# Optimization experiments

Measured on AMD Instinct MI355X. Metric: run time of the kernel, lower is better.

The kernel has to match this reference:

```python
import jax, jax.numpy as jnp
import numpy as np

N_ITER = 3

def setup_inputs() -> dict:
    key = jax.random.key(0)
    k1, k2 = jax.random.split(key)
    x = jax.random.normal(k1, (8, 1024, 512), dtype=jnp.float32)
    W = jax.random.normal(k2, (4, 512, 512), dtype=jnp.float32)
    return {"x": x, "W": W}

def reference(x, W):
    # x: [B, N, D], W: [H, D, D]
    B, N, D = x.shape
    H = W.shape[0]
    scale = D ** (-0.5)
    logits = jnp.zeros((B, H, N, N), dtype=x.dtype)
    rw = None
    for _ in range(N_ITER):
        rw = jax.nn.softmax(logits, axis=-1)              # [B, H, N, N]
        # per-head bilinear scores: (x @ W_h) @ x^T * scale, batched over heads
        logits = jnp.einsum('bnd,hde,bme->bhnm', x, W, x) * scale
    # routing_weights @ x, then mean over heads -> [B, N, D]
    out = jnp.einsum('bhnm,bmd->bhnd', rw, x)
    return jnp.mean(out, axis=1)
```

## Files before the change

kernel.cpp:

```cpp
#include <hip/hip_runtime.h>
#include <math.h>

#define B_ 8
#define N_ 1024
#define D_ 512
#define H_ 4
#define ND (N_ * D_)
#define DD (D_ * D_)
#define NN (N_ * N_)

typedef _Float16 f16;
typedef f16 f16x8 __attribute__((ext_vector_type(8)));
typedef float f32x4 __attribute__((ext_vector_type(4)));

typedef __attribute__((address_space(3))) void lds_void;
typedef __attribute__((address_space(1))) void g_void;


#define MFMA16(QR, QC, AV, BV)                                                \
    _Pragma("unroll")                                                         \
    for (int i_ = 0; i_ < 4; ++i_)                                            \
        _Pragma("unroll")                                                     \
        for (int j_ = 0; j_ < 2; ++j_) {                                      \
            acc[(QR)*4+i_][(QC)*2+j_] = __builtin_amdgcn_mfma_f32_16x16x32_f16(AV[i_][0], BV[j_][0], acc[(QR)*4+i_][(QC)*2+j_], 0, 0, 0); \
            acc[(QR)*4+i_][(QC)*2+j_] = __builtin_amdgcn_mfma_f32_16x16x32_f16(AV[i_][1], BV[j_][1], acc[(QR)*4+i_][(QC)*2+j_], 0, 0, 0); \
        }

#define READ_A(AV, PA, HALF)                                                  \
    _Pragma("unroll")                                                         \
    for (int i_ = 0; i_ < 4; ++i_) {                                          \
        const int ra_ = (HALF) * 128 + wr * 64 + i_ * 16 + fr;                \
        AV[i_][0] = *(const f16x8*)(PA + ra_ * 64 + sw0 * 8);                 \
        AV[i_][1] = *(const f16x8*)(PA + ra_ * 64 + sw1 * 8);                 \
    }

#define READ_B(BV, PB, HALF)                                                  \
    _Pragma("unroll")                                                         \
    for (int j_ = 0; j_ < 2; ++j_) {                                          \
        const int rb_ = (HALF) * 128 + wc * 32 + j_ * 16 + fr;                \
        BV[j_][0] = *(const f16x8*)(PB + rb_ * 64 + sw0 * 8);                 \
        BV[j_][1] = *(const f16x8*)(PB + rb_ * 64 + sw1 * 8);                 \
    }

#define PHASE_SYNC_MFMA(QR, QC, AV, BV, STAGE, TAIL)                          \
    __builtin_amdgcn_sched_barrier(0);                                        \
    STAGE;                                                                    \
    __builtin_amdgcn_s_barrier();                                             \
    asm volatile("s_waitcnt lgkmcnt(0)" ::: "memory");                        \
    __builtin_amdgcn_sched_barrier(0);                                        \
    __builtin_amdgcn_s_setprio(1);                                            \
    MFMA16(QR, QC, AV, BV);                                                   \
    __builtin_amdgcn_s_setprio(0);                                            \
    TAIL;                                                                     \
    __builtin_amdgcn_s_barrier();

template<int LDA, int LDB, int LDC, int KTOT>
__device__ __forceinline__ void gemm256(
    const f16* __restrict__ A, const f16* __restrict__ B,
    f16* __restrict__ C, float scale, int m0, int n0)
{
    constexpr int NT = KTOT / 64;
    __shared__ f16 sA0[256 * 64];
    __shared__ f16 sB0[256 * 64];
    __shared__ f16 sA1[256 * 64];
    __shared__ f16 sB1[256 * 64];

    const int t = threadIdx.x;
    const int w = t >> 6, l = t & 63;
    const int fr = l & 15, fq = l >> 4;
    const int wr = w >> 2, wc = w & 3;
    const int lr = l >> 3, lc = l & 7;
    const int swc = lc ^ lr;
    const int sw0 = fq ^ (fr & 7);
    const int sw1 = (4 + fq) ^ (fr & 7);

    f32x4 acc[8][4] = {};

    auto stageA = [&](f16* buf, int half, int kt) {
#pragma unroll
        for (int i = 0; i < 2; ++i) {
            const int r0 = half * 128 + i * 64 + w * 8;
            const f16* g = A + (size_t)(m0 + r0 + lr) * LDA + kt * 64 + swc * 8;
            __builtin_amdgcn_global_load_lds((g_void*)g, (lds_void*)(buf + r0 * 64), 16, 0, 0);
        }
    };
    auto stageB = [&](f16* buf, int half, int kt) {
#pragma unroll
        for (int i = 0; i < 2; ++i) {
            const int r0 = half * 128 + i * 64 + w * 8;
            const f16* g = B + (size_t)(n0 + r0 + lr) * LDB + kt * 64 + swc * 8;
            __builtin_amdgcn_global_load_lds((g_void*)g, (lds_void*)(buf + r0 * 64), 16, 0, 0);
        }
    };

    stageA(sA0, 0, 0); stageB(sB0, 0, 0);
    stageA(sA0, 1, 0); stageB(sB0, 1, 0);
    if (NT > 1) { stageA(sA1, 0, 1); stageB(sB1, 0, 1); }
    asm volatile("s_waitcnt vmcnt(4)" ::: "memory");
    __builtin_amdgcn_s_barrier();

#pragma unroll
    for (int kt = 0; kt < NT; ++kt) {
        f16* cA = (kt & 1) ? sA1 : sA0;
        f16* cB = (kt & 1) ? sB1 : sB0;
        f16* nA = (kt & 1) ? sA0 : sA1;
        f16* nB = (kt & 1) ? sB0 : sB1;

        f16x8 av0[4][2], av1[4][2], bv0[2][2], bv1[2][2];

        READ_A(av0, cA, 0);
        READ_B(bv0, cB, 0);
        PHASE_SYNC_MFMA(0, 0, av0, bv0,
            { if (kt + 1 < NT) stageA(nA, 1, kt + 1); }, {});

        READ_B(bv1, cB, 1);
        PHASE_SYNC_MFMA(0, 1, av0, bv1,
            { if (kt + 1 < NT) stageB(nB, 1, kt + 1); }, {});

        READ_A(av1, cA, 1);
        PHASE_SYNC_MFMA(1, 1, av1, bv1,
            { if (kt + 2 < NT) stageA(cA, 0, kt + 2); }, {});

        PHASE_SYNC_MFMA(1, 0, av1, bv0,
            { if (kt + 2 < NT) stageB(cB, 0, kt + 2); },
            { if (kt + 2 < NT) { asm volatile("s_waitcnt vmcnt(4)" ::: "memory"); }
              else             { asm volatile("s_waitcnt vmcnt(0)" ::: "memory"); } });
    }

#pragma unroll
    for (int ri = 0; ri < 8; ++ri)
#pragma unroll
        for (int cj = 0; cj < 4; ++cj)
#pragma unroll
            for (int rr = 0; rr < 4; ++rr) {
                const int row = m0 + (ri >> 2) * 128 + wr * 64 + (ri & 3) * 16 + fq * 4 + rr;
                const int col = n0 + (cj >> 1) * 128 + wc * 32 + (cj & 1) * 16 + fr;
                C[(size_t)row * LDC + col] = (f16)(acc[ri][cj][rr] * scale);
            }
}

__global__ __launch_bounds__(512, 2) void k_g1(
    const f16* __restrict__ xfh, const f16* __restrict__ wTh,
    f16* __restrict__ Yh)
{
    const int i = blockIdx.x;
    const int b = i & 7;
    const int li = i >> 3;
    const int h = li >> 3;
    const int tile = li & 7;
    const int m0 = (tile >> 1) * 256;
    const int n0 = (tile & 1) * 256;
    const int z = b * 4 + h;
    gemm256<D_, D_, D_, D_>(
        xfh + (size_t)b * ND,
        wTh + (size_t)h * DD,
        Yh + (size_t)z * ND, 1.0f, m0, n0);
}

__global__ __launch_bounds__(512, 2) void k_g2(
    const f16* __restrict__ Yh, const f16* __restrict__ xfh,
    f16* __restrict__ S)
{
    const int i = blockIdx.x;
    const int b = i & 7;
    const int li = i >> 3;
    const int h = li >> 4;
    const int tile = li & 15;
    const int m0 = (tile >> 2) * 256;
    const int n0 = (tile & 3) * 256;
    const int z = b * 4 + h;
    gemm256<D_, D_, N_, D_>(
        Yh + (size_t)z * ND,
        xfh + (size_t)b * ND,
        S + (size_t)z * NN, 0.044194173824159216f, m0, n0);
}

__global__ __launch_bounds__(512, 2) void k_g4(
    const f16* __restrict__ P, const f16* __restrict__ xT,
    f16* __restrict__ part)
{
    const int i = blockIdx.x;
    const int b = i & 7;
    const int li = i >> 3;
    const int h = li >> 3;
    const int tile = li & 7;
    const int m0 = (tile >> 1) * 256;
    const int n0 = (tile & 1) * 256;
    const int z = b * 4 + h;
    gemm256<N_, N_, D_, N_>(
        P + (size_t)z * NN,
        xT + (size_t)b * ND,
        part + (size_t)z * ND, 1.0f, m0, n0);
}

__global__ __launch_bounds__(256) void k_reduce(
    const f16* __restrict__ part, float* __restrict__ out)
{
    const int i = blockIdx.x * 256 + threadIdx.x;
    const int b = i / (ND / 8);
    const int r = i - b * (ND / 8);
    const f16x8* p = (const f16x8*)part;
    f16x8 a0 = p[(size_t)(b * 4 + 0) * (ND / 8) + r];
    f16x8 a1 = p[(size_t)(b * 4 + 1) * (ND / 8) + r];
    f16x8 a2 = p[(size_t)(b * 4 + 2) * (ND / 8) + r];
    f16x8 a3 = p[(size_t)(b * 4 + 3) * (ND / 8) + r];
    float4 o0, o1;
    float* o = (float*)&o0;
#pragma unroll
    for (int k = 0; k < 4; ++k)
        o[k] = 0.25f * ((float)a0[k] + (float)a1[k] + (float)a2[k] + (float)a3[k]);
    o = (float*)&o1;
#pragma unroll
    for (int k = 0; k < 4; ++k)
        o[k] = 0.25f * ((float)a0[k+4] + (float)a1[k+4] + (float)a2[k+4] + (float)a3[k+4]);
    ((float4*)out)[(size_t)i * 2]     = o0;
    ((float4*)out)[(size_t)i * 2 + 1] = o1;
}

__global__ __launch_bounds__(256) void decomp_xw(
    const float* __restrict__ x, const float* __restrict__ W,
    f16* __restrict__ xfh, f16* __restrict__ xT, f16* __restrict__ wTh)
{
    __shared__ f16 tile[64][65];
    __shared__ float tw[64][65];
    const int t = threadIdx.x;
    const int z = blockIdx.z;
    if (z < 8) {
        const int b = z, n0 = blockIdx.y * 64, d0 = blockIdx.x * 64;
        const float* xb = x + (size_t)b * ND;
#pragma unroll
        for (int p = 0; p < 16; ++p) {
            const int idx = t + p * 256;
            const int r = idx >> 6, c = idx & 63;
            const float v = xb[(size_t)(n0 + r) * D_ + d0 + c];
            const f16 h = (f16)v;
            xfh[(size_t)b * ND + (size_t)(n0 + r) * D_ + d0 + c] = h;
            tile[r][c] = h;
        }
        __syncthreads();
#pragma unroll
        for (int p = 0; p < 16; ++p) {
            const int idx = t + p * 256;
            const int r = idx >> 6, c = idx & 63;
            xT[(size_t)b * ND + (size_t)(d0 + r) * N_ + n0 + c] = tile[c][r];
        }
    } else {
        if (blockIdx.y >= 8) return;
        const int h = z - 8, d0 = blockIdx.y * 64, e0 = blockIdx.x * 64;
        const float* Wh = W + (size_t)h * DD;
#pragma unroll
        for (int p = 0; p < 16; ++p) {
            const int idx = t + p * 256;
            const int r = idx >> 6, c = idx & 63;
            tw[r][c] = Wh[(size_t)(d0 + r) * D_ + e0 + c];
        }
        __syncthreads();
#pragma unroll
        for (int p = 0; p < 16; ++p) {
            const int idx = t + p * 256;
            const int r = idx >> 6, c = idx & 63;
            wTh[(size_t)h * DD + (size_t)(e0 + r) * D_ + d0 + c] = (f16)tw[c][r];
        }
    }
}

__global__ __launch_bounds__(256) void softmax_wave(
    const f16* __restrict__ S, f16* __restrict__ P)
{
    const int wave = threadIdx.x >> 6;
    const int l = threadIdx.x & 63;
    const int i = blockIdx.x;
    const int b = i & 7;
    const int li = i >> 3;
    const int h = li >> 8;
    const int rg = li & 255;
    const size_t row = (size_t)(b * 4 + h) * N_ + rg * 4 + wave;

    const f16x8* p = (const f16x8*)(S + row * N_);
    f16x8 v0 = p[l * 2], v1 = p[l * 2 + 1];

    float f[16];
#pragma unroll
    for (int k = 0; k < 8; ++k) { f[k] = (float)v0[k]; f[k + 8] = (float)v1[k]; }

    float m = f[0];
#pragma unroll
    for (int k = 1; k < 16; ++k) m = fmaxf(m, f[k]);
#pragma unroll
    for (int o = 32; o > 0; o >>= 1) m = fmaxf(m, __shfl_xor(m, o));

    float s = 0.f;
#pragma unroll
    for (int k = 0; k < 16; ++k) { f[k] = __expf(f[k] - m); s += f[k]; }
#pragma unroll
    for (int o = 32; o > 0; o >>= 1) s += __shfl_xor(s, o);

    const float inv = 1.0f / s;
    f16x8 o0, o1;
#pragma unroll
    for (int k = 0; k < 8; ++k) {
        o0[k] = (f16)(f[k] * inv);
        o1[k] = (f16)(f[k + 8] * inv);
    }
    f16x8* q = (f16x8*)(P + row * N_);
    q[l * 2] = o0;
    q[l * 2 + 1] = o1;
}

extern "C" void kernel_launch(void* const* d_in, const int* in_sizes, int n_in,
                              void* d_out, int out_size, void* d_ws, size_t ws_size,
                              hipStream_t stream) {
    const float* x = (const float*)d_in[0];
    const float* W = (const float*)d_in[1];
    float* out = (float*)d_out;

    char* ws = (char*)d_ws;
    const size_t MB = 1024 * 1024;
    f16*   xfh = (f16*)(ws + 0 * MB);
    f16*   xT  = (f16*)(ws + 8 * MB);
    f16*   wTh = (f16*)(ws + 16 * MB);
    f16*   Yh  = (f16*)(ws + 20 * MB);
    f16*   S   = (f16*)(ws + 52 * MB);
    f16*   P   = (f16*)(ws + 116 * MB);
    f16*   part = S;

    decomp_xw<<<dim3(8, 16, 12), 256, 0, stream>>>(x, W, xfh, xT, wTh);

    k_g1<<<dim3(256), 512, 0, stream>>>(xfh, wTh, Yh);
    k_g2<<<dim3(512), 512, 0, stream>>>(Yh, xfh, S);
    softmax_wave<<<dim3(B_ * H_ * N_ / 4), 256, 0, stream>>>(S, P);
    k_g4<<<dim3(256), 512, 0, stream>>>(P, xT, part);
    k_reduce<<<dim3((B_ * ND / 8) / 256), 256, 0, stream>>>(part, out);
}
```

Before: 190.3 us.

## Average softmax over heads before final GEMM and drop reduce kernel

```diff
diff --git a/kernel.cpp b/kernel.cpp
--- a/kernel.cpp
+++ b/kernel.cpp
@@ -136,6 +136,64 @@
                 const int row = m0 + (ri >> 2) * 128 + wr * 64 + (ri & 3) * 16 + fq * 4 + rr;
                 const int col = n0 + (cj >> 1) * 128 + wc * 32 + (cj & 1) * 16 + fr;
                 C[(size_t)row * LDC + col] = (f16)(acc[ri][cj][rr] * scale);
+            }
+}
+
+template<int LDA, int LDB, int LDC, int KTOT>
+__device__ __forceinline__ void single_core_f32(
+    const f16* __restrict__ A, const f16* __restrict__ B0,
+    float* __restrict__ C, int n0, int c0)
+{
+    __shared__ f16 sA[128 * 32];
+    __shared__ f16 sB0[128 * 32];
+
+    const int t = threadIdx.x;
+    const int w = t >> 6;
+    const int l = t & 63;
+    const int lrow = l >> 2;
+    const int lch  = l & 3;
+    const int wr = w >> 1, wc = w & 1;
+    const int fr = l & 15;
+    const int fq = l >> 4;
+
+    f32x4 acc[4][4] = {};
+
+    for (int k0 = 0; k0 < KTOT; k0 += 32) {
+#pragma unroll
+        for (int i = 0; i < 2; ++i) {
+            const int rb  = w * 2 + i;
+            const int row = rb * 16 + lrow;
+            const f16* ga = A + (size_t)(n0 + row) * LDA + k0 + lch * 8;
+            __builtin_amdgcn_global_load_lds((g_void*)ga, (lds_void*)(sA + rb * 512), 16, 0, 0);
+            const f16* gb0 = B0 + (size_t)(c0 + row) * LDB + k0 + lch * 8;
+            __builtin_amdgcn_global_load_lds((g_void*)gb0, (lds_void*)(sB0 + rb * 512), 16, 0, 0);
+        }
+        __syncthreads();
+
+        f16x8 a[4], b0[4];
+#pragma unroll
+        for (int i = 0; i < 4; ++i) {
+            a[i]  = *(const f16x8*)(sA  + (wr * 64 + i * 16 + fr) * 32 + fq * 8);
+            b0[i] = *(const f16x8*)(sB0 + (wc * 64 + i * 16 + fr) * 32 + fq * 8);
+        }
+
+#pragma unroll
+        for (int i = 0; i < 4; ++i)
+#pragma unroll
+            for (int j = 0; j < 4; ++j)
+                acc[i][j] = __builtin_amdgcn_mfma_f32_16x16x32_f16(a[i], b0[j], acc[i][j], 0, 0, 0);
+        __syncthreads();
+    }
+
+#pragma unroll
+    for (int i = 0; i < 4; ++i)
+#pragma unroll
+        for (int j = 0; j < 4; ++j)
+#pragma unroll
+            for (int r = 0; r < 4; ++r) {
+                const int row = n0 + wr * 64 + i * 16 + fq * 4 + r;
+                const int col = c0 + wc * 64 + j * 16 + fr;
+                C[(size_t)row * LDC + col] = acc[i][j][r];
             }
 }
 
@@ -175,46 +233,63 @@
         S + (size_t)z * NN, 0.044194173824159216f, m0, n0);
 }
 
-__global__ __launch_bounds__(512, 2) void k_g4(
-    const f16* __restrict__ P, const f16* __restrict__ xT,
-    f16* __restrict__ part)
+__global__ __launch_bounds__(256) void softmax_mean(
+    const f16* __restrict__ S, f16* __restrict__ Pb)
+{
+    const int wave = threadIdx.x >> 6;
+    const int l = threadIdx.x & 63;
+    const int i = blockIdx.x;
+    const int b = i & 7;
+    const int rg = i >> 3;
+    const int row = rg * 4 + wave;
+
+    float o[16];
+#pragma unroll
+    for (int k = 0; k < 16; ++k) o[k] = 0.f;
+
+#pragma unroll
+    for (int h = 0; h < 4; ++h) {
+        const f16x8* p = (const f16x8*)(S + ((size_t)(b * 4 + h) * N_ + row) * N_);
+        f16x8 v0 = p[l * 2], v1 = p[l * 2 + 1];
+        float f[16];
+#pragma unroll
+        for (int k = 0; k < 8; ++k) { f[k] = (float)v0[k]; f[k + 8] = (float)v1[k]; }
+        float m = f[0];
+#pragma unroll
+        for (int k = 1; k < 16; ++k) m = fmaxf(m, f[k]);
+#pragma unroll
+        for (int off = 32; off > 0; off >>= 1) m = fmaxf(m, __shfl_xor(m, off));
+        float s = 0.f;
+#pragma unroll
+        for (int k = 0; k < 16; ++k) { f[k] = __expf(f[k] - m); s += f[k]; }
+#pragma unroll
+        for (int off = 32; off > 0; off >>= 1) s += __shfl_xor(s, off);
+        const float q = 0.25f / s;
+#pragma unroll
+        for (int k = 0; k < 16; ++k) o[k] += f[k] * q;
+    }
+
+    f16x8 o0, o1;
+#pragma unroll
+    for (int k = 0; k < 8; ++k) { o0[k] = (f16)o[k]; o1[k] = (f16)o[k + 8]; }
+    f16x8* qp = (f16x8*)(Pb + ((size_t)b * N_ + row) * N_);
+    qp[l * 2] = o0;
+    qp[l * 2 + 1] = o1;
+}
+
+__global__ __launch_bounds__(256, 2) void k_g4b(
+    const f16* __restrict__ Pb, const f16* __restrict__ xT,
+    float* __restrict__ out)
 {
     const int i = blockIdx.x;
     const int b = i & 7;
     const int li = i >> 3;
-    const int h = li >> 3;
-    const int tile = li & 7;
-    const int m0 = (tile >> 1) * 256;
-    const int n0 = (tile & 1) * 256;
-    const int z = b * 4 + h;
-    gemm256<N_, N_, D_, N_>(
-        P + (size_t)z * NN,
+    const int m0 = (li >> 2) * 128;
+    const int d0 = (li & 3) * 128;
+    single_core_f32<N_, N_, D_, N_>(
+        Pb + (size_t)b * NN,
         xT + (size_t)b * ND,
-        part + (size_t)z * ND, 1.0f, m0, n0);
-}
-
-__global__ __launch_bounds__(256) void k_reduce(
-    const f16* __restrict__ part, float* __restrict__ out)
-{
-    const int i = blockIdx.x * 256 + threadIdx.x;
-    const int b = i / (ND / 8);
-    const int r = i - b * (ND / 8);
-    const f16x8* p = (const f16x8*)part;
-    f16x8 a0 = p[(size_t)(b * 4 + 0) * (ND / 8) + r];
-    f16x8 a1 = p[(size_t)(b * 4 + 1) * (ND / 8) + r];
-    f16x8 a2 = p[(size_t)(b * 4 + 2) * (ND / 8) + r];
-    f16x8 a3 = p[(size_t)(b * 4 + 3) * (ND / 8) + r];
-    float4 o0, o1;
-    float* o = (float*)&o0;
-#pragma unroll
-    for (int k = 0; k < 4; ++k)
-        o[k] = 0.25f * ((float)a0[k] + (float)a1[k] + (float)a2[k] + (float)a3[k]);
-    o = (float*)&o1;
-#pragma unroll
-    for (int k = 0; k < 4; ++k)
-        o[k] = 0.25f * ((float)a0[k+4] + (float)a1[k+4] + (float)a2[k+4] + (float)a3[k+4]);
-    ((float4*)out)[(size_t)i * 2]     = o0;
-    ((float4*)out)[(size_t)i * 2 + 1] = o1;
+        out + (size_t)b * ND, m0, d0);
 }
 
 __global__ __launch_bounds__(256) void decomp_xw(
@@ -264,49 +339,6 @@
     }
 }
 
-__global__ __launch_bounds__(256) void softmax_wave(
-    const f16* __restrict__ S, f16* __restrict__ P)
-{
-    const int wave = threadIdx.x >> 6;
-    const int l = threadIdx.x & 63;
-    const int i = blockIdx.x;
-    const int b = i & 7;
-    const int li = i >> 3;
-    const int h = li >> 8;
-    const int rg = li & 255;
-    const size_t row = (size_t)(b * 4 + h) * N_ + rg * 4 + wave;
-
-    const f16x8* p = (const f16x8*)(S + row * N_);
-    f16x8 v0 = p[l * 2], v1 = p[l * 2 + 1];
-
-    float f[16];
-#pragma unroll
-    for (int k = 0; k < 8; ++k) { f[k] = (float)v0[k]; f[k + 8] = (float)v1[k]; }
-
-    float m = f[0];
-#pragma unroll
-    for (int k = 1; k < 16; ++k) m = fmaxf(m, f[k]);
-#pragma unroll
-    for (int o = 32; o > 0; o >>= 1) m = fmaxf(m, __shfl_xor(m, o));
-
-    float s = 0.f;
-#pragma unroll
-    for (int k = 0; k < 16; ++k) { f[k] = __expf(f[k] - m); s += f[k]; }
-#pragma unroll
-    for (int o = 32; o > 0; o >>= 1) s += __shfl_xor(s, o);
-
-    const float inv = 1.0f / s;
-    f16x8 o0, o1;
-#pragma unroll
-    for (int k = 0; k < 8; ++k) {
-        o0[k] = (f16)(f[k] * inv);
-        o1[k] = (f16)(f[k + 8] * inv);
-    }
-    f16x8* q = (f16x8*)(P + row * N_);
-    q[l * 2] = o0;
-    q[l * 2 + 1] = o1;
-}
-
 extern "C" void kernel_launch(void* const* d_in, const int* in_sizes, int n_in,
                               void* d_out, int out_size, void* d_ws, size_t ws_size,
                               hipStream_t stream) {
@@ -321,14 +353,12 @@
     f16*   wTh = (f16*)(ws + 16 * MB);
     f16*   Yh  = (f16*)(ws + 20 * MB);
     f16*   S   = (f16*)(ws + 52 * MB);
-    f16*   P   = (f16*)(ws + 116 * MB);
-    f16*   part = S;
+    f16*   Pb  = (f16*)(ws + 116 * MB);
 
     decomp_xw<<<dim3(8, 16, 12), 256, 0, stream>>>(x, W, xfh, xT, wTh);
 
     k_g1<<<dim3(256), 512, 0, stream>>>(xfh, wTh, Yh);
     k_g2<<<dim3(512), 512, 0, stream>>>(Yh, xfh, S);
-    softmax_wave<<<dim3(B_ * H_ * N_ / 4), 256, 0, stream>>>(S, P);
-    k_g4<<<dim3(256), 512, 0, stream>>>(P, xT, part);
-    k_reduce<<<dim3((B_ * ND / 8) / 256), 256, 0, stream>>>(part, out);
-}
+    softmax_mean<<<dim3(2048), 256, 0, stream>>>(S, Pb);
+    k_g4b<<<dim3(256), 256, 0, stream>>>(Pb, xT, out);
+}
```

Result: faster. 171.3 us (-10.0%).
